# Performance work log

Hardware: AMD Instinct MI355X
Metric: run time of the kernel (lower is better)

The kernel has to match this reference:

```python
import jax, jax.numpy as jnp
import numpy as np

N, C, NS = 131072, 128, 16
BN_EPS = 1e-5


def setup_inputs() -> dict:
    key = jax.random.key(0)
    ks = jax.random.split(key, 8)
    p = jax.random.normal(ks[0], (N, 3), dtype=jnp.float32)
    u = jax.random.normal(ks[1], (N, C), dtype=jnp.float32)
    o = jnp.array([N], dtype=jnp.int32)  # batch offset (single cloud)
    idx = jax.random.randint(ks[2], (N, NS), 0, N, dtype=jnp.int32)  # precomputed KNN indices
    s = 1.0 / np.sqrt(C)
    W1 = jax.random.uniform(ks[3], (C, C), jnp.float32, -s, s)
    b1 = jax.random.uniform(ks[4], (C,), jnp.float32, -s, s)
    W2 = jax.random.uniform(ks[5], (C, C), jnp.float32, -s, s)
    b2 = jax.random.uniform(ks[6], (C,), jnp.float32, -s, s)
    gamma = jnp.ones((C,), jnp.float32)
    beta = jnp.zeros((C,), jnp.float32)
    return {"p": p, "u": u, "o": o, "idx": idx, "W1": W1, "b1": b1,
            "W2": W2, "b2": b2, "gamma": gamma, "beta": beta}


def reference(p, u, o, idx, W1, b1, W2, b2, gamma, beta):
    # pre_trans: Linear(d_in, d_in)
    u_pre = u @ W1 + b1                                  # [N, C]
    # queryandgroup (use_xyz=False): gather neighbor features by KNN idx
    u_n = u_pre[idx]                                     # [N, NS, C] irregular gather
    # local Laplacian: ReLU(neighbor - center), mean over neighborhood
    lap = jnp.maximum(u_n - u_pre[:, None, :], 0.0).mean(axis=1)  # [N, C]
    # varphi: Linear -> BatchNorm1d (training stats) -> ReLU
    h = lap @ W2 + b2                                    # [N, C]
    mean = h.mean(axis=0)
    var = ((h - mean) ** 2).mean(axis=0)  # biased var, as BN normalization uses
    h = (h - mean) * jax.lax.rsqrt(var + BN_EPS) * gamma + beta
    u_tt = jnp.maximum(h, 0.0)
    return (p, u_tt, o)
```

## Files before the change

### kernel.cpp

```cpp
#include <hip/hip_runtime.h>

#define N_PTS 131072
#define C_DIM 128
#define NS_K  16
#define BN_EPS 1e-5f

typedef unsigned short ushort_t;
typedef unsigned short u16x8 __attribute__((ext_vector_type(8)));
typedef __bf16 bf16x8 __attribute__((ext_vector_type(8)));
typedef float f32x4 __attribute__((ext_vector_type(4)));

__device__ __forceinline__ ushort_t f2b(float f) {
    unsigned int u = __float_as_uint(f);
    u += 0x7FFFu + ((u >> 16) & 1u);
    return (ushort_t)(u >> 16);
}
__device__ __forceinline__ float b2f(ushort_t h) {
    return __uint_as_float((unsigned int)h << 16);
}

template <bool A_BF16, bool STATS>
__global__ __launch_bounds__(256) void gemm_mfma_kernel(
    const void* __restrict__ Aptr, const float* __restrict__ W,
    const float* __restrict__ bias, ushort_t* __restrict__ out,
    float* __restrict__ gsum, float* __restrict__ gsq)
{
    __shared__ __align__(16) ushort_t a_sh[128 * 136];
    __shared__ __align__(16) ushort_t w_sh[128 * 136];
    __shared__ float s_sum[128];
    __shared__ float s_sq[128];

    const int tid = threadIdx.x;
    const int base = blockIdx.x * 128;

    if (STATS && tid < 128) { s_sum[tid] = 0.f; s_sq[tid] = 0.f; }

    {
        const int row  = tid >> 1;
        const int half = (tid & 1) * 64;
        ushort_t* as = a_sh + row * 136 + half;
        if (A_BF16) {
            const ushort_t* ag = (const ushort_t*)Aptr + (size_t)(base + row) * 128 + half;
            #pragma unroll
            for (int j = 0; j < 8; j++)
                *(u16x8*)(as + j * 8) = *(const u16x8*)(ag + j * 8);
        } else {
            const float* ag = (const float*)Aptr + (size_t)(base + row) * 128 + half;
            #pragma unroll
            for (int j = 0; j < 8; j++) {
                f32x4 lo = *(const f32x4*)(ag + j * 8);
                f32x4 hi = *(const f32x4*)(ag + j * 8 + 4);
                u16x8 v;
                v[0] = f2b(lo[0]); v[1] = f2b(lo[1]); v[2] = f2b(lo[2]); v[3] = f2b(lo[3]);
                v[4] = f2b(hi[0]); v[5] = f2b(hi[1]); v[6] = f2b(hi[2]); v[7] = f2b(hi[3]);
                *(u16x8*)(as + j * 8) = v;
            }
        }
    }
    {
        const int n  = tid & 127;
        const int kb = (tid >> 7) * 64;
        #pragma unroll 8
        for (int k = 0; k < 64; k++)
            w_sh[n * 136 + kb + k] = f2b(W[(kb + k) * 128 + n]);
    }
    __syncthreads();

    const int lane = tid & 63;
    const int wv   = tid >> 6;
    const int m16  = lane & 15;
    const int q    = lane >> 4;

    f32x4 acc[2][8];
    #pragma unroll
    for (int i = 0; i < 2; i++)
        #pragma unroll
        for (int c = 0; c < 8; c++) acc[i][c] = (f32x4){0.f, 0.f, 0.f, 0.f};

    const ushort_t* ap0 = a_sh + ((wv * 2 + 0) * 16 + m16) * 136 + q * 8;
    const ushort_t* ap1 = a_sh + ((wv * 2 + 1) * 16 + m16) * 136 + q * 8;
    const ushort_t* wp  = w_sh + m16 * 136 + q * 8;

    #pragma unroll
    for (int k0 = 0; k0 < 128; k0 += 32) {
        bf16x8 a0 = __builtin_bit_cast(bf16x8, *(const u16x8*)(ap0 + k0));
        bf16x8 a1 = __builtin_bit_cast(bf16x8, *(const u16x8*)(ap1 + k0));
        #pragma unroll
        for (int c = 0; c < 8; c++) {
            bf16x8 b = __builtin_bit_cast(bf16x8, *(const u16x8*)(wp + c * (16 * 136) + k0));
            acc[0][c] = __builtin_amdgcn_mfma_f32_16x16x32_bf16(a0, b, acc[0][c], 0, 0, 0);
            acc[1][c] = __builtin_amdgcn_mfma_f32_16x16x32_bf16(a1, b, acc[1][c], 0, 0, 0);
        }
    }

    float psum[8], psq[8];
    #pragma unroll
    for (int c = 0; c < 8; c++) { psum[c] = 0.f; psq[c] = 0.f; }

    #pragma unroll
    for (int c = 0; c < 8; c++) {
        const int col = c * 16 + m16;
        const float bv = bias[col];
        #pragma unroll
        for (int i = 0; i < 2; i++) {
            const int rb = base + (wv * 2 + i) * 16 + q * 4;
            #pragma unroll
            for (int r = 0; r < 4; r++) {
                const float v = acc[i][c][r] + bv;
                out[(size_t)(rb + r) * 128 + col] = f2b(v);
                if (STATS) { psum[c] += v; psq[c] += v * v; }
            }
        }
    }

    if (STATS) {
        #pragma unroll
        for (int c = 0; c < 8; c++) {
            atomicAdd(&s_sum[c * 16 + m16], psum[c]);
            atomicAdd(&s_sq[c * 16 + m16],  psq[c]);
        }
        __syncthreads();
        if (tid < 128) {
            atomicAdd(&gsum[tid], s_sum[tid]);
            atomicAdd(&gsq[tid],  s_sq[tid]);
        }
    }
}

__global__ __launch_bounds__(256) void laplacian_kernel(
    const ushort_t* __restrict__ table, const int* __restrict__ idx,
    ushort_t* __restrict__ lap)
{
    __shared__ int s_idx[256];
    const int tid = threadIdx.x;
    s_idx[tid] = idx[blockIdx.x * 256 + tid];
    __syncthreads();

    const int p  = tid >> 4;
    const int c8 = (tid & 15) * 8;
    const size_t pt = (size_t)blockIdx.x * 16 + p;

    const u16x8 cv = *(const u16x8*)(table + pt * 128 + c8);
    float ctr[8];
    #pragma unroll
    for (int e = 0; e < 8; e++) ctr[e] = b2f(cv[e]);

    float acc[8];
    #pragma unroll
    for (int e = 0; e < 8; e++) acc[e] = 0.f;

    #pragma unroll
    for (int s = 0; s < NS_K; s++) {
        const int j = s_idx[p * 16 + s];
        const u16x8 nv = *(const u16x8*)(table + (size_t)j * 128 + c8);
        #pragma unroll
        for (int e = 0; e < 8; e++)
            acc[e] += fmaxf(b2f(nv[e]) - ctr[e], 0.f);
    }

    u16x8 o;
    #pragma unroll
    for (int e = 0; e < 8; e++) o[e] = f2b(acc[e] * (1.f / (float)NS_K));
    *(u16x8*)(lap + pt * 128 + c8) = o;
}

__global__ void bn_stats_kernel(const float* __restrict__ gsum,
                                const float* __restrict__ gsq,
                                const float* __restrict__ gamma,
                                const float* __restrict__ beta,
                                float* __restrict__ bnsc, float* __restrict__ bnsh)
{
    const int c = threadIdx.x;
    const float invN = 1.f / (float)N_PTS;
    const float mean = gsum[c] * invN;
    const float var  = gsq[c] * invN - mean * mean;
    const float sc   = rsqrtf(var + BN_EPS) * gamma[c];
    bnsc[c] = sc;
    bnsh[c] = fmaf(-mean, sc, beta[c]);
}

__global__ __launch_bounds__(256) void bn_relu_kernel(
    const ushort_t* __restrict__ h, const float* __restrict__ bnsc,
    const float* __restrict__ bnsh, float* __restrict__ out)
{
    const size_t i = (size_t)blockIdx.x * 256 + threadIdx.x;
    const int c8 = (threadIdx.x * 8) & 127;

    const u16x8 hv = *(const u16x8*)(h + i * 8);
    const f32x4 sc0 = *(const f32x4*)(bnsc + c8);
    const f32x4 sc1 = *(const f32x4*)(bnsc + c8 + 4);
    const f32x4 sh0 = *(const f32x4*)(bnsh + c8);
    const f32x4 sh1 = *(const f32x4*)(bnsh + c8 + 4);

    f32x4 o0, o1;
    #pragma unroll
    for (int e = 0; e < 4; e++) {
        o0[e] = fmaxf(fmaf(b2f(hv[e]),     sc0[e], sh0[e]), 0.f);
        o1[e] = fmaxf(fmaf(b2f(hv[4 + e]), sc1[e], sh1[e]), 0.f);
    }
    float* op = out + (size_t)3 * N_PTS + i * 8;
    *(f32x4*)(op)     = o0;
    *(f32x4*)(op + 4) = o1;
}

__global__ __launch_bounds__(256) void copy_p_kernel(
    const float* __restrict__ p, const int* __restrict__ o,
    float* __restrict__ out)
{
    const size_t i = (size_t)blockIdx.x * 256 + threadIdx.x;
    *(f32x4*)(out + i * 4) = *(const f32x4*)(p + i * 4);
    if (i == 0)
        out[(size_t)3 * N_PTS + (size_t)N_PTS * C_DIM] = (float)o[0];
}

extern "C" void kernel_launch(void* const* d_in, const int* in_sizes, int n_in,
                              void* d_out, int out_size, void* d_ws, size_t ws_size,
                              hipStream_t stream) {
    const float* p     = (const float*)d_in[0];
    const float* u     = (const float*)d_in[1];
    const int*   o     = (const int*)d_in[2];
    const int*   idx   = (const int*)d_in[3];
    const float* W1    = (const float*)d_in[4];
    const float* b1    = (const float*)d_in[5];
    const float* W2    = (const float*)d_in[6];
    const float* b2    = (const float*)d_in[7];
    const float* gamma = (const float*)d_in[8];
    const float* beta  = (const float*)d_in[9];
    float* out = (float*)d_out;

    char* ws = (char*)d_ws;
    const size_t buf_bytes = (size_t)N_PTS * C_DIM * sizeof(ushort_t);
    ushort_t* table = (ushort_t*)ws;
    ushort_t* lap   = (ushort_t*)(ws + buf_bytes);
    ushort_t* h     = (ushort_t*)(ws + 2 * buf_bytes);
    float*    stats = (float*)(ws + 3 * buf_bytes);
    float* gsum = stats;
    float* gsq  = stats + 128;
    float* bnsc = stats + 256;
    float* bnsh = stats + 384;

    hipMemsetAsync(stats, 0, 256 * sizeof(float), stream);

    gemm_mfma_kernel<false, false><<<N_PTS / 128, 256, 0, stream>>>(
        u, W1, b1, table, nullptr, nullptr);
    laplacian_kernel<<<N_PTS / 16, 256, 0, stream>>>(table, idx, lap);
    gemm_mfma_kernel<true, true><<<N_PTS / 128, 256, 0, stream>>>(
        lap, W2, b2, h, gsum, gsq);
    bn_stats_kernel<<<1, 128, 0, stream>>>(gsum, gsq, gamma, beta, bnsc, bnsh);
    bn_relu_kernel<<<(N_PTS * C_DIM / 8) / 256, 256, 0, stream>>>(
        h, bnsc, bnsh, out);
    copy_p_kernel<<<(3 * N_PTS / 4) / 256, 256, 0, stream>>>(p, o, out);
}
```

Baseline: 297.7 us.

## Pre-transpose weights to bf16 once and read GEMM operands directly from global

Adds a small kernel that converts and transposes W1 and W2 to bf16 once per call, so each GEMM block no longer does the strided fp32 transpose-and-convert of the full weight matrix. The GEMM kernel also drops its shared-memory staging of A and W and loads MFMA fragments straight from global memory (weights served from cache). This removes the per-block LDS fill and barrier and frees LDS for occupancy, at the cost of less coalesced per-lane global loads and repeated weight reads through L1/L2.

```diff
diff --git a/kernel.cpp b/kernel.cpp
--- a/kernel.cpp
+++ b/kernel.cpp
@@ -19,57 +19,40 @@
     return __uint_as_float((unsigned int)h << 16);
 }
 
+__global__ __launch_bounds__(256) void prep_w_kernel(
+    const float* __restrict__ W1, const float* __restrict__ W2,
+    ushort_t* __restrict__ wT1, ushort_t* __restrict__ wT2)
+{
+    const int t = blockIdx.x * 256 + threadIdx.x;
+    const int n = t & 127;
+    const int k = t >> 7;
+    wT1[n * 128 + k] = f2b(W1[k * 128 + n]);
+    wT2[n * 128 + k] = f2b(W2[k * 128 + n]);
+}
+
 template <bool A_BF16, bool STATS>
 __global__ __launch_bounds__(256) void gemm_mfma_kernel(
-    const void* __restrict__ Aptr, const float* __restrict__ W,
+    const void* __restrict__ Aptr, const ushort_t* __restrict__ wT,
     const float* __restrict__ bias, ushort_t* __restrict__ out,
     float* __restrict__ gsum, float* __restrict__ gsq)
 {
-    __shared__ __align__(16) ushort_t a_sh[128 * 136];
-    __shared__ __align__(16) ushort_t w_sh[128 * 136];
     __shared__ float s_sum[128];
     __shared__ float s_sq[128];
 
-    const int tid = threadIdx.x;
-    const int base = blockIdx.x * 128;
-
-    if (STATS && tid < 128) { s_sum[tid] = 0.f; s_sq[tid] = 0.f; }
-
-    {
-        const int row  = tid >> 1;
-        const int half = (tid & 1) * 64;
-        ushort_t* as = a_sh + row * 136 + half;
-        if (A_BF16) {
-            const ushort_t* ag = (const ushort_t*)Aptr + (size_t)(base + row) * 128 + half;
-            #pragma unroll
-            for (int j = 0; j < 8; j++)
-                *(u16x8*)(as + j * 8) = *(const u16x8*)(ag + j * 8);
-        } else {
-            const float* ag = (const float*)Aptr + (size_t)(base + row) * 128 + half;
-            #pragma unroll
-            for (int j = 0; j < 8; j++) {
-                f32x4 lo = *(const f32x4*)(ag + j * 8);
-                f32x4 hi = *(const f32x4*)(ag + j * 8 + 4);
-                u16x8 v;
-                v[0] = f2b(lo[0]); v[1] = f2b(lo[1]); v[2] = f2b(lo[2]); v[3] = f2b(lo[3]);
-                v[4] = f2b(hi[0]); v[5] = f2b(hi[1]); v[6] = f2b(hi[2]); v[7] = f2b(hi[3]);
-                *(u16x8*)(as + j * 8) = v;
-            }
-        }
-    }
-    {
-        const int n  = tid & 127;
-        const int kb = (tid >> 7) * 64;
-        #pragma unroll 8
-        for (int k = 0; k < 64; k++)
-            w_sh[n * 136 + kb + k] = f2b(W[(kb + k) * 128 + n]);
-    }
-    __syncthreads();
-
+    const int tid  = threadIdx.x;
     const int lane = tid & 63;
     const int wv   = tid >> 6;
     const int m16  = lane & 15;
     const int q    = lane >> 4;
+    const int base = blockIdx.x * 128;
+
+    if (STATS) {
+        if (tid < 128) { s_sum[tid] = 0.f; s_sq[tid] = 0.f; }
+        __syncthreads();
+    }
+
+    const size_t row0 = (size_t)base + (wv * 2 + 0) * 16 + m16;
+    const size_t row1 = (size_t)base + (wv * 2 + 1) * 16 + m16;
 
     f32x4 acc[2][8];
     #pragma unroll
@@ -77,17 +60,33 @@
         #pragma unroll
         for (int c = 0; c < 8; c++) acc[i][c] = (f32x4){0.f, 0.f, 0.f, 0.f};
 
-    const ushort_t* ap0 = a_sh + ((wv * 2 + 0) * 16 + m16) * 136 + q * 8;
-    const ushort_t* ap1 = a_sh + ((wv * 2 + 1) * 16 + m16) * 136 + q * 8;
-    const ushort_t* wp  = w_sh + m16 * 136 + q * 8;
-
     #pragma unroll
     for (int k0 = 0; k0 < 128; k0 += 32) {
-        bf16x8 a0 = __builtin_bit_cast(bf16x8, *(const u16x8*)(ap0 + k0));
-        bf16x8 a1 = __builtin_bit_cast(bf16x8, *(const u16x8*)(ap1 + k0));
+        const int koff = q * 8 + k0;
+        bf16x8 a0, a1;
+        if (A_BF16) {
+            const ushort_t* ab = (const ushort_t*)Aptr;
+            a0 = __builtin_bit_cast(bf16x8, *(const u16x8*)(ab + row0 * 128 + koff));
+            a1 = __builtin_bit_cast(bf16x8, *(const u16x8*)(ab + row1 * 128 + koff));
+        } else {
+            const float* af = (const float*)Aptr;
+            const f32x4 l0 = *(const f32x4*)(af + row0 * 128 + koff);
+            const f32x4 h0 = *(const f32x4*)(af + row0 * 128 + koff + 4);
+            const f32x4 l1 = *(const f32x4*)(af + row1 * 128 + koff);
+            const f32x4 h1 = *(const f32x4*)(af + row1 * 128 + koff + 4);
+            u16x8 v0, v1;
+            #pragma unroll
+            for (int e = 0; e < 4; e++) {
+                v0[e] = f2b(l0[e]); v0[4 + e] = f2b(h0[e]);
+                v1[e] = f2b(l1[e]); v1[4 + e] = f2b(h1[e]);
+            }
+            a0 = __builtin_bit_cast(bf16x8, v0);
+            a1 = __builtin_bit_cast(bf16x8, v1);
+        }
         #pragma unroll
         for (int c = 0; c < 8; c++) {
-            bf16x8 b = __builtin_bit_cast(bf16x8, *(const u16x8*)(wp + c * (16 * 136) + k0));
+            const bf16x8 b = __builtin_bit_cast(bf16x8,
+                *(const u16x8*)(wT + (size_t)(c * 16 + m16) * 128 + koff));
             acc[0][c] = __builtin_amdgcn_mfma_f32_16x16x32_bf16(a0, b, acc[0][c], 0, 0, 0);
             acc[1][c] = __builtin_amdgcn_mfma_f32_16x16x32_bf16(a1, b, acc[1][c], 0, 0, 0);
         }
@@ -238,14 +237,17 @@
     float* gsq  = stats + 128;
     float* bnsc = stats + 256;
     float* bnsh = stats + 384;
+    ushort_t* wT1 = (ushort_t*)(stats + 512);
+    ushort_t* wT2 = wT1 + 128 * 128;
 
     hipMemsetAsync(stats, 0, 256 * sizeof(float), stream);
 
+    prep_w_kernel<<<64, 256, 0, stream>>>(W1, W2, wT1, wT2);
     gemm_mfma_kernel<false, false><<<N_PTS / 128, 256, 0, stream>>>(
-        u, W1, b1, table, nullptr, nullptr);
+        u, wT1, b1, table, nullptr, nullptr);
     laplacian_kernel<<<N_PTS / 16, 256, 0, stream>>>(table, idx, lap);
     gemm_mfma_kernel<true, true><<<N_PTS / 128, 256, 0, stream>>>(
-        lap, W2, b2, h, gsum, gsq);
+        lap, wT2, b2, h, gsum, gsq);
     bn_stats_kernel<<<1, 128, 0, stream>>>(gsum, gsq, gamma, beta, bnsc, bnsh);
     bn_relu_kernel<<<(N_PTS * C_DIM / 8) / 256, 256, 0, stream>>>(
         h, bnsc, bnsh, out);
```

Measured after the change: 322.6 us. 8.4% more time.

## Pre-transpose weights to bf16 once and stage GEMM output through LDS

Applied to the files above, without the earlier changes.

Adds a small kernel that converts and transposes W1/W2 to bf16 once, so each GEMM block loads weights with vectorized 16-byte copies instead of per-block strided fp32 loads plus conversion. The GEMM epilogue now writes results into shared memory and then stores them to global memory as coalesced 16-byte rows, replacing scattered 2-byte stores. This costs an extra kernel launch, a bit of workspace, and an additional barrier.

```diff
diff --git a/kernel.cpp b/kernel.cpp
--- a/kernel.cpp
+++ b/kernel.cpp
@@ -19,9 +19,20 @@
     return __uint_as_float((unsigned int)h << 16);
 }
 
+__global__ __launch_bounds__(256) void prep_w_kernel(
+    const float* __restrict__ W1, const float* __restrict__ W2,
+    ushort_t* __restrict__ wT1, ushort_t* __restrict__ wT2)
+{
+    const int t = blockIdx.x * 256 + threadIdx.x;
+    const int n = t & 127;
+    const int k = t >> 7;
+    wT1[n * 128 + k] = f2b(W1[k * 128 + n]);
+    wT2[n * 128 + k] = f2b(W2[k * 128 + n]);
+}
+
 template <bool A_BF16, bool STATS>
 __global__ __launch_bounds__(256) void gemm_mfma_kernel(
-    const void* __restrict__ Aptr, const float* __restrict__ W,
+    const void* __restrict__ Aptr, const ushort_t* __restrict__ wT,
     const float* __restrict__ bias, ushort_t* __restrict__ out,
     float* __restrict__ gsum, float* __restrict__ gsq)
 {
@@ -30,7 +41,11 @@
     __shared__ float s_sum[128];
     __shared__ float s_sq[128];
 
-    const int tid = threadIdx.x;
+    const int tid  = threadIdx.x;
+    const int lane = tid & 63;
+    const int wv   = tid >> 6;
+    const int m16  = lane & 15;
+    const int q    = lane >> 4;
     const int base = blockIdx.x * 128;
 
     if (STATS && tid < 128) { s_sum[tid] = 0.f; s_sq[tid] = 0.f; }
@@ -58,18 +73,15 @@
         }
     }
     {
-        const int n  = tid & 127;
-        const int kb = (tid >> 7) * 64;
-        #pragma unroll 8
-        for (int k = 0; k < 64; k++)
-            w_sh[n * 136 + kb + k] = f2b(W[(kb + k) * 128 + n]);
-    }
-    __syncthreads();
-
-    const int lane = tid & 63;
-    const int wv   = tid >> 6;
-    const int m16  = lane & 15;
-    const int q    = lane >> 4;
+        const int n    = tid >> 1;
+        const int half = (tid & 1) * 64;
+        const ushort_t* wg = wT + (size_t)n * 128 + half;
+        ushort_t* ws = w_sh + n * 136 + half;
+        #pragma unroll
+        for (int j = 0; j < 8; j++)
+            *(u16x8*)(ws + j * 8) = *(const u16x8*)(wg + j * 8);
+    }
+    __syncthreads();
 
     f32x4 acc[2][8];
     #pragma unroll
@@ -93,6 +105,8 @@
         }
     }
 
+    __syncthreads();
+
     float psum[8], psq[8];
     #pragma unroll
     for (int c = 0; c < 8; c++) { psum[c] = 0.f; psq[c] = 0.f; }
@@ -103,27 +117,37 @@
         const float bv = bias[col];
         #pragma unroll
         for (int i = 0; i < 2; i++) {
-            const int rb = base + (wv * 2 + i) * 16 + q * 4;
+            const int rb = (wv * 2 + i) * 16 + q * 4;
             #pragma unroll
             for (int r = 0; r < 4; r++) {
                 const float v = acc[i][c][r] + bv;
-                out[(size_t)(rb + r) * 128 + col] = f2b(v);
+                a_sh[(rb + r) * 136 + col] = f2b(v);
                 if (STATS) { psum[c] += v; psq[c] += v * v; }
             }
         }
     }
-
     if (STATS) {
         #pragma unroll
         for (int c = 0; c < 8; c++) {
             atomicAdd(&s_sum[c * 16 + m16], psum[c]);
             atomicAdd(&s_sq[c * 16 + m16],  psq[c]);
         }
-        __syncthreads();
-        if (tid < 128) {
-            atomicAdd(&gsum[tid], s_sum[tid]);
-            atomicAdd(&gsq[tid],  s_sq[tid]);
-        }
+    }
+    __syncthreads();
+
+    {
+        const int r0 = tid >> 4;
+        const int c0 = (tid & 15) * 8;
+        #pragma unroll
+        for (int it = 0; it < 8; it++) {
+            const int rl = r0 + it * 16;
+            const u16x8 v = *(const u16x8*)(a_sh + rl * 136 + c0);
+            *(u16x8*)(out + (size_t)(base + rl) * 128 + c0) = v;
+        }
+    }
+    if (STATS && tid < 128) {
+        atomicAdd(&gsum[tid], s_sum[tid]);
+        atomicAdd(&gsq[tid],  s_sq[tid]);
     }
 }
 
@@ -238,14 +262,17 @@
     float* gsq  = stats + 128;
     float* bnsc = stats + 256;
     float* bnsh = stats + 384;
+    ushort_t* wT1 = (ushort_t*)(stats + 512);
+    ushort_t* wT2 = wT1 + 128 * 128;
 
     hipMemsetAsync(stats, 0, 256 * sizeof(float), stream);
 
+    prep_w_kernel<<<64, 256, 0, stream>>>(W1, W2, wT1, wT2);
     gemm_mfma_kernel<false, false><<<N_PTS / 128, 256, 0, stream>>>(
-        u, W1, b1, table, nullptr, nullptr);
+        u, wT1, b1, table, nullptr, nullptr);
     laplacian_kernel<<<N_PTS / 16, 256, 0, stream>>>(table, idx, lap);
     gemm_mfma_kernel<true, true><<<N_PTS / 128, 256, 0, stream>>>(
-        lap, W2, b2, h, gsum, gsq);
+        lap, wT2, b2, h, gsum, gsq);
     bn_stats_kernel<<<1, 128, 0, stream>>>(gsum, gsq, gamma, beta, bnsc, bnsh);
     bn_relu_kernel<<<(N_PTS * C_DIM / 8) / 256, 256, 0, stream>>>(
         h, bnsc, bnsh, out);
```

Measured after the change: 288.3 us. 1.03x faster.
